# Performance work log

Hardware: AMD Instinct MI355X
Metric: run time of the kernel (lower is better)

Reference implementation:

```python
import math
import jax, jax.numpy as jnp
import numpy as np

B, L, D, H = 4, 512, 256, 8
DH = D // H
BUCKETS = 11  # rel_pos_buckets; padding_idx = BUCKETS


def setup_inputs() -> dict:
    key = jax.random.key(0)
    ks = jax.random.split(key, 12)
    s = 0.02
    rel_table = jax.random.normal(ks[10], (BUCKETS + 1, D), dtype=jnp.float32) * s
    rel_table = rel_table.at[BUCKETS].set(0.0)  # padding_idx row is zero
    return {
        "inputs": jax.random.normal(ks[0], (B, L, D), dtype=jnp.float32),
        "mask": jax.random.randint(ks[1], (B, L, L), 0, 2) > 0,
        "distances": jax.random.randint(ks[2], (B, L, L), 0, BUCKETS + 1),
        "Wq": jax.random.normal(ks[3], (D, D), dtype=jnp.float32) * s,
        "bq": jnp.zeros((D,), jnp.float32),
        "Wk": jax.random.normal(ks[4], (D, D), dtype=jnp.float32) * s,
        "bk": jnp.zeros((D,), jnp.float32),
        "Wv": jax.random.normal(ks[5], (D, D), dtype=jnp.float32) * s,
        "bv": jnp.zeros((D,), jnp.float32),
        "Wo": jax.random.normal(ks[6], (D, D), dtype=jnp.float32) * s,
        "bo": jnp.zeros((D,), jnp.float32),
        "rel_table": rel_table,
        "u": jax.random.normal(ks[7], (D,), dtype=jnp.float32) * s,
        "v": jax.random.normal(ks[8], (D,), dtype=jnp.float32) * s,
    }


def reference(inputs, mask, distances, Wq, bq, Wk, bk, Wv, bv, Wo, bo, rel_table, u, v):
    def shape(x):  # (B, L, D) -> (B, H, L, DH)
        return x.reshape(B, L, H, DH).transpose(0, 2, 1, 3)

    q = shape(inputs @ Wq + bq) / math.sqrt(DH)
    k = shape(inputs @ Wk + bk)
    val = shape(inputs @ Wv + bv)

    # content term: (q + u) k^T
    a_c = jnp.einsum("bhqd,bhkd->bhqk", q + u.reshape(1, H, 1, DH), k)

    # relative-position term: embedding gather (padding row already zero, mask anyway)
    valid = (distances != BUCKETS)[..., None].astype(rel_table.dtype)
    rel = (rel_table[distances] * valid).reshape(B, L, L, H, DH)  # (B, Lq, Lk, H, DH)
    b_d = jnp.einsum("bhqd,bqkhd->bhqk", q + v.reshape(1, H, 1, DH), rel)

    scores = jnp.where(mask[:, None, :, :], jnp.float32(-1e18), a_c + b_d)
    attn = jax.nn.softmax(scores, axis=-1)  # (B, H, Lq, Lk)

    ctx = jnp.einsum("bhqk,bhkd->bhqd", attn, val)
    ctx = ctx.transpose(0, 2, 1, 3).reshape(B, L, D)
    output = ctx @ Wo + bo
    return output, attn
```

## Files before the change

kernel.cpp:

```cpp
#include <hip/hip_runtime.h>
#include <math.h>

#define BB 4
#define LL 512
#define DD 256
#define HH 8
#define DHH 32
#define NB 12

__global__ __launch_bounds__(256) void qkv_kernel(const float* __restrict__ x,
    const float* __restrict__ Wq, const float* __restrict__ bq,
    const float* __restrict__ Wk, const float* __restrict__ bk,
    const float* __restrict__ Wv, const float* __restrict__ bv,
    const float* __restrict__ uvec, const float* __restrict__ vvec,
    float* __restrict__ Qu, float* __restrict__ Qv,
    float* __restrict__ KT, float* __restrict__ V) {
    __shared__ float xs[8][DD];
    const int mat = blockIdx.x >> 8;
    const int r0 = (blockIdx.x & 255) * 8;
    const int t = threadIdx.x;
    const int cg = t & 63, rg = t >> 6;
    const int c0 = cg * 4;
    {
        const float4* xg = (const float4*)(x + r0 * DD);
        float4* xsv = (float4*)&xs[0][0];
        xsv[t] = xg[t];
        xsv[t + 256] = xg[t + 256];
    }
    __syncthreads();
    const float* W    = (mat == 0) ? Wq : (mat == 1) ? Wk : Wv;
    const float* bias = (mat == 0) ? bq : (mat == 1) ? bk : bv;
    float acc[2][4];
#pragma unroll
    for (int r = 0; r < 2; ++r)
#pragma unroll
        for (int c = 0; c < 4; ++c) acc[r][c] = bias[c0 + c];
    for (int i0 = 0; i0 < DD; i0 += 4) {
        float4 wv4[4], xv4[2];
#pragma unroll
        for (int j = 0; j < 4; ++j) wv4[j] = *(const float4*)&W[(i0 + j) * DD + c0];
#pragma unroll
        for (int r = 0; r < 2; ++r) xv4[r] = *(const float4*)&xs[rg * 2 + r][i0];
        const float* wf = (const float*)wv4;
        const float* xf = (const float*)xv4;
#pragma unroll
        for (int r = 0; r < 2; ++r)
#pragma unroll
            for (int j = 0; j < 4; ++j)
#pragma unroll
                for (int c = 0; c < 4; ++c)
                    acc[r][c] = fmaf(xf[r * 4 + j], wf[j * 4 + c], acc[r][c]);
    }
    if (mat == 0) {
        const float s = 0.17677669529663687f;
        const float4 u4 = *(const float4*)&uvec[c0];
        const float4 v4 = *(const float4*)&vvec[c0];
#pragma unroll
        for (int r = 0; r < 2; ++r) {
            const int row = r0 + rg * 2 + r;
            float4 q = make_float4(acc[r][0] * s, acc[r][1] * s, acc[r][2] * s, acc[r][3] * s);
            *(float4*)&Qu[row * DD + c0] = make_float4(q.x + u4.x, q.y + u4.y, q.z + u4.z, q.w + u4.w);
            *(float4*)&Qv[row * DD + c0] = make_float4(q.x + v4.x, q.y + v4.y, q.z + v4.z, q.w + v4.w);
        }
    } else if (mat == 1) {
        const int b = r0 >> 9;
        const int kb = (r0 & 511) + rg * 2;
#pragma unroll
        for (int c = 0; c < 4; ++c) {
            const int col = c0 + c;
            const int h = col >> 5, dd = col & 31;
            float* p = KT + ((long)((b * HH + h) * DHH + dd)) * LL + kb;
            p[0] = acc[0][c];
            p[1] = acc[1][c];
        }
    } else {
#pragma unroll
        for (int r = 0; r < 2; ++r)
            *(float4*)&V[(r0 + rg * 2 + r) * DD + c0] =
                make_float4(acc[r][0], acc[r][1], acc[r][2], acc[r][3]);
    }
}

__global__ __launch_bounds__(512, 4) void scores_ctx_kernel(const float* __restrict__ Qu,
    const float* __restrict__ Qv, const float* __restrict__ KT,
    const float* __restrict__ rel_table, const int* __restrict__ mask,
    const int* __restrict__ dist, const float* __restrict__ V,
    float* __restrict__ attn, float* __restrict__ ctx) {
    __shared__ float Qs[16][DHH];
    __shared__ float Qv8[16][DHH];
    __shared__ float rels[NB][DHH + 1];
    __shared__ float Ps[16][NB];
    __shared__ float Ss[16][4][132];
    __shared__ float Vs[DHH][133];
    const int blk = blockIdx.x;
    const int h = blk & 7;
    const int rest = blk >> 3;
    const int qt = rest & 31;
    const int b = rest >> 5;
    const int q0 = qt * 16;
    const int t = threadIdx.x;
    const int w = t >> 6, l = t & 63;

    {
        const int r = t >> 5, c = t & 31;
        Qs[r][c]  = Qu[(b * LL + q0 + r) * DD + h * DHH + c];
        Qv8[r][c] = Qv[(b * LL + q0 + r) * DD + h * DHH + c];
    }
    if (t < NB * DHH) {
        rels[t >> 5][t & 31] = rel_table[(t >> 5) * DD + h * DHH + (t & 31)];
    }
    __syncthreads();
    if (t < 16 * NB) {
        const int bk = t >> 4, r = t & 15;
        float a = 0.f;
#pragma unroll
        for (int d = 0; d < DHH; ++d) a = fmaf(Qv8[r][d], rels[bk][d], a);
        Ps[r][bk] = a;
    }
    __syncthreads();

    const int r0 = 2 * w;
    const long kbase = (long)(b * HH + h) * DHH * LL;
    float e0[2][4], e1[2][4];
    float sum0 = 0.f, sum1 = 0.f;
#pragma unroll
    for (int s = 0; s < 2; ++s) {
        const int k0 = 4 * l + 256 * s;
        const int4 dx0 = *(const int4*)&dist[(b * LL + q0 + r0) * LL + k0];
        const int4 dx1 = *(const int4*)&dist[(b * LL + q0 + r0 + 1) * LL + k0];
        const int4 mx0 = *(const int4*)&mask[(b * LL + q0 + r0) * LL + k0];
        const int4 mx1 = *(const int4*)&mask[(b * LL + q0 + r0 + 1) * LL + k0];
        float s0[4], s1[4];
        s0[0] = Ps[r0][dx0.x]; s0[1] = Ps[r0][dx0.y]; s0[2] = Ps[r0][dx0.z]; s0[3] = Ps[r0][dx0.w];
        s1[0] = Ps[r0 + 1][dx1.x]; s1[1] = Ps[r0 + 1][dx1.y]; s1[2] = Ps[r0 + 1][dx1.z]; s1[3] = Ps[r0 + 1][dx1.w];
#pragma unroll
        for (int d8 = 0; d8 < DHH; d8 += 8) {
            float4 kv[8];
#pragma unroll
            for (int j = 0; j < 8; ++j)
                kv[j] = *(const float4*)&KT[kbase + (long)(d8 + j) * LL + k0];
            const float4 q0a = *(const float4*)&Qs[r0][d8];
            const float4 q0b = *(const float4*)&Qs[r0][d8 + 4];
            const float4 q1a = *(const float4*)&Qs[r0 + 1][d8];
            const float4 q1b = *(const float4*)&Qs[r0 + 1][d8 + 4];
            const float* qa0 = (const float*)&q0a;
            const float* qb0 = (const float*)&q0b;
            const float* qa1 = (const float*)&q1a;
            const float* qb1 = (const float*)&q1b;
#pragma unroll
            for (int j = 0; j < 4; ++j) {
                s0[0] = fmaf(qa0[j], kv[j].x, s0[0]);
                s0[1] = fmaf(qa0[j], kv[j].y, s0[1]);
                s0[2] = fmaf(qa0[j], kv[j].z, s0[2]);
                s0[3] = fmaf(qa0[j], kv[j].w, s0[3]);
                s1[0] = fmaf(qa1[j], kv[j].x, s1[0]);
                s1[1] = fmaf(qa1[j], kv[j].y, s1[1]);
                s1[2] = fmaf(qa1[j], kv[j].z, s1[2]);
                s1[3] = fmaf(qa1[j], kv[j].w, s1[3]);
            }
#pragma unroll
            for (int j = 0; j < 4; ++j) {
                s0[0] = fmaf(qb0[j], kv[j + 4].x, s0[0]);
                s0[1] = fmaf(qb0[j], kv[j + 4].y, s0[1]);
                s0[2] = fmaf(qb0[j], kv[j + 4].z, s0[2]);
                s0[3] = fmaf(qb0[j], kv[j + 4].w, s0[3]);
                s1[0] = fmaf(qb1[j], kv[j + 4].x, s1[0]);
                s1[1] = fmaf(qb1[j], kv[j + 4].y, s1[1]);
                s1[2] = fmaf(qb1[j], kv[j + 4].z, s1[2]);
                s1[3] = fmaf(qb1[j], kv[j + 4].w, s1[3]);
            }
        }
        e0[s][0] = mx0.x ? 0.f : __expf(s0[0]);
        e0[s][1] = mx0.y ? 0.f : __expf(s0[1]);
        e0[s][2] = mx0.z ? 0.f : __expf(s0[2]);
        e0[s][3] = mx0.w ? 0.f : __expf(s0[3]);
        e1[s][0] = mx1.x ? 0.f : __expf(s1[0]);
        e1[s][1] = mx1.y ? 0.f : __expf(s1[1]);
        e1[s][2] = mx1.z ? 0.f : __expf(s1[2]);
        e1[s][3] = mx1.w ? 0.f : __expf(s1[3]);
        sum0 += (e0[s][0] + e0[s][1]) + (e0[s][2] + e0[s][3]);
        sum1 += (e1[s][0] + e1[s][1]) + (e1[s][2] + e1[s][3]);
    }
    for (int off = 32; off > 0; off >>= 1) {
        sum0 += __shfl_xor(sum0, off);
        sum1 += __shfl_xor(sum1, off);
    }
    const float i0 = 1.0f / sum0, i1 = 1.0f / sum1;
    float* a0 = attn + ((long)(b * HH + h) * LL + q0 + r0) * LL;
    float* a1 = a0 + LL;
#pragma unroll
    for (int s = 0; s < 2; ++s) {
        const int k0 = 4 * l + 256 * s;
        const int ch = k0 >> 7, off = k0 & 127;
        const float4 o0 = make_float4(e0[s][0] * i0, e0[s][1] * i0, e0[s][2] * i0, e0[s][3] * i0);
        const float4 o1 = make_float4(e1[s][0] * i1, e1[s][1] * i1, e1[s][2] * i1, e1[s][3] * i1);
        *(float4*)&a0[k0] = o0;
        *(float4*)&a1[k0] = o1;
        *(float4*)&Ss[r0][ch][off] = o0;
        *(float4*)&Ss[r0 + 1][ch][off] = o1;
    }

    const int qB = t >> 5;
    const int dB = t & 31;
    const int kkS = t >> 2;
    const int dqS = (t & 3) * 8;
    float acc = 0.f;
    for (int c = 0; c < 4; ++c) {
        __syncthreads();
        {
            const float* vg = V + ((long)(b * LL + c * 128 + kkS)) * DD + h * DHH + dqS;
            const float4 va = *(const float4*)&vg[0];
            const float4 vb4 = *(const float4*)&vg[4];
            Vs[dqS + 0][kkS] = va.x;  Vs[dqS + 1][kkS] = va.y;
            Vs[dqS + 2][kkS] = va.z;  Vs[dqS + 3][kkS] = va.w;
            Vs[dqS + 4][kkS] = vb4.x; Vs[dqS + 5][kkS] = vb4.y;
            Vs[dqS + 6][kkS] = vb4.z; Vs[dqS + 7][kkS] = vb4.w;
        }
        __syncthreads();
#pragma unroll
        for (int j = 0; j < 32; ++j) {
            const float4 sv = *(const float4*)&Ss[qB][c][4 * j];
            const float4 vv = *(const float4*)&Vs[dB][4 * j];
            acc = fmaf(sv.x, vv.x, fmaf(sv.y, vv.y, fmaf(sv.z, vv.z, fmaf(sv.w, vv.w, acc))));
        }
    }
    ctx[(b * LL + q0 + qB) * DD + h * DHH + dB] = acc;
}

__global__ __launch_bounds__(256) void outproj_kernel(const float* __restrict__ ctx,
    const float* __restrict__ Wo, const float* __restrict__ bo,
    float* __restrict__ out) {
    __shared__ float xs[4][DD];
    const int r0 = blockIdx.x * 4;
    const int t = threadIdx.x;
    const int rg = t >> 6;
    const int c0 = (t & 63) * 4;
    ((float4*)&xs[0][0])[t] = ((const float4*)(ctx + r0 * DD))[t];
    __syncthreads();
    float4 acc = *(const float4*)&bo[c0];
    for (int i0 = 0; i0 < DD; i0 += 8) {
        float4 wv[8];
#pragma unroll
        for (int j = 0; j < 8; ++j) wv[j] = *(const float4*)&Wo[(i0 + j) * DD + c0];
        const float4 x0 = *(const float4*)&xs[rg][i0];
        const float4 x1 = *(const float4*)&xs[rg][i0 + 4];
        const float* xf0 = (const float*)&x0;
        const float* xf1 = (const float*)&x1;
#pragma unroll
        for (int j = 0; j < 4; ++j) {
            acc.x = fmaf(xf0[j], wv[j].x, acc.x);
            acc.y = fmaf(xf0[j], wv[j].y, acc.y);
            acc.z = fmaf(xf0[j], wv[j].z, acc.z);
            acc.w = fmaf(xf0[j], wv[j].w, acc.w);
        }
#pragma unroll
        for (int j = 0; j < 4; ++j) {
            acc.x = fmaf(xf1[j], wv[j + 4].x, acc.x);
            acc.y = fmaf(xf1[j], wv[j + 4].y, acc.y);
            acc.z = fmaf(xf1[j], wv[j + 4].z, acc.z);
            acc.w = fmaf(xf1[j], wv[j + 4].w, acc.w);
        }
    }
    *(float4*)&out[(r0 + rg) * DD + c0] = acc;
}

extern "C" void kernel_launch(void* const* d_in, const int* in_sizes, int n_in,
                              void* d_out, int out_size, void* d_ws, size_t ws_size,
                              hipStream_t stream) {
    const float* x    = (const float*)d_in[0];
    const int* mk     = (const int*)d_in[1];
    const int* dist   = (const int*)d_in[2];
    const float* Wq = (const float*)d_in[3];
    const float* bq = (const float*)d_in[4];
    const float* Wk = (const float*)d_in[5];
    const float* bk = (const float*)d_in[6];
    const float* Wv = (const float*)d_in[7];
    const float* bv = (const float*)d_in[8];
    const float* Wo = (const float*)d_in[9];
    const float* bo = (const float*)d_in[10];
    const float* rel_table = (const float*)d_in[11];
    const float* uvec = (const float*)d_in[12];
    const float* vvec = (const float*)d_in[13];

    float* out  = (float*)d_out;
    float* attn = out + BB * LL * DD;

    float* Qu = (float*)d_ws;
    float* Qv = Qu + BB * LL * DD;
    float* KT = Qv + BB * LL * DD;
    float* V  = KT + BB * LL * DD;
    float* C  = V + BB * LL * DD;

    qkv_kernel<<<3 * 256, 256, 0, stream>>>(x, Wq, bq, Wk, bk, Wv, bv, uvec, vvec,
                                            Qu, Qv, KT, V);
    scores_ctx_kernel<<<BB * (LL / 16) * HH, 512, 0, stream>>>(Qu, Qv, KT, rel_table,
                                                               mk, dist, V, attn, C);
    outproj_kernel<<<BB * LL / 4, 256, 0, stream>>>(C, Wo, bo, out);
}
```

Baseline: 179.3 us.

## Register-tile P·V with split-K across threads and XOR-swizzled score buffer

```diff
diff --git a/kernel.cpp b/kernel.cpp
--- a/kernel.cpp
+++ b/kernel.cpp
@@ -87,97 +87,108 @@
     const int* __restrict__ dist, const float* __restrict__ V,
     float* __restrict__ attn, float* __restrict__ ctx) {
     __shared__ float Qs[16][DHH];
-    __shared__ float Qv8[16][DHH];
-    __shared__ float rels[NB][DHH + 1];
     __shared__ float Ps[16][NB];
-    __shared__ float Ss[16][4][132];
+    __shared__ float ss[16 * 512];
     __shared__ float Vs[DHH][133];
     const int blk = blockIdx.x;
     const int h = blk & 7;
     const int rest = blk >> 3;
-    const int qt = rest & 31;
+    const int qt16 = rest & 31;
     const int b = rest >> 5;
-    const int q0 = qt * 16;
+    const int q0 = qt16 * 16;
     const int t = threadIdx.x;
     const int w = t >> 6, l = t & 63;
 
+    float* Qv8  = ss;
+    float* rels = ss + 512;
+
     {
         const int r = t >> 5, c = t & 31;
-        Qs[r][c]  = Qu[(b * LL + q0 + r) * DD + h * DHH + c];
-        Qv8[r][c] = Qv[(b * LL + q0 + r) * DD + h * DHH + c];
+        Qs[r][c]          = Qu[(b * LL + q0 + r) * DD + h * DHH + c];
+        Qv8[r * DHH + c]  = Qv[(b * LL + q0 + r) * DD + h * DHH + c];
     }
     if (t < NB * DHH) {
-        rels[t >> 5][t & 31] = rel_table[(t >> 5) * DD + h * DHH + (t & 31)];
+        rels[(t >> 5) * 33 + (t & 31)] = rel_table[(t >> 5) * DD + h * DHH + (t & 31)];
     }
     __syncthreads();
     if (t < 16 * NB) {
         const int bk = t >> 4, r = t & 15;
         float a = 0.f;
 #pragma unroll
-        for (int d = 0; d < DHH; ++d) a = fmaf(Qv8[r][d], rels[bk][d], a);
+        for (int d = 0; d < DHH; ++d) a = fmaf(Qv8[r * DHH + d], rels[bk * 33 + d], a);
         Ps[r][bk] = a;
     }
     __syncthreads();
 
     const int r0 = 2 * w;
     const long kbase = (long)(b * HH + h) * DHH * LL;
-    float e0[2][4], e1[2][4];
-    float sum0 = 0.f, sum1 = 0.f;
+    float sc[2][2][4];
 #pragma unroll
     for (int s = 0; s < 2; ++s) {
         const int k0 = 4 * l + 256 * s;
         const int4 dx0 = *(const int4*)&dist[(b * LL + q0 + r0) * LL + k0];
         const int4 dx1 = *(const int4*)&dist[(b * LL + q0 + r0 + 1) * LL + k0];
+        sc[0][s][0] = Ps[r0][dx0.x];     sc[0][s][1] = Ps[r0][dx0.y];
+        sc[0][s][2] = Ps[r0][dx0.z];     sc[0][s][3] = Ps[r0][dx0.w];
+        sc[1][s][0] = Ps[r0 + 1][dx1.x]; sc[1][s][1] = Ps[r0 + 1][dx1.y];
+        sc[1][s][2] = Ps[r0 + 1][dx1.z]; sc[1][s][3] = Ps[r0 + 1][dx1.w];
+    }
+#pragma unroll
+    for (int d8 = 0; d8 < DHH; d8 += 8) {
+        const float4 q0a = *(const float4*)&Qs[r0][d8];
+        const float4 q0b = *(const float4*)&Qs[r0][d8 + 4];
+        const float4 q1a = *(const float4*)&Qs[r0 + 1][d8];
+        const float4 q1b = *(const float4*)&Qs[r0 + 1][d8 + 4];
+        const float* qa0 = (const float*)&q0a;
+        const float* qb0 = (const float*)&q0b;
+        const float* qa1 = (const float*)&q1a;
+        const float* qb1 = (const float*)&q1b;
+#pragma unroll
+        for (int s = 0; s < 2; ++s) {
+            const int k0 = 4 * l + 256 * s;
+            float4 kv[8];
+#pragma unroll
+            for (int j = 0; j < 8; ++j)
+                kv[j] = *(const float4*)&KT[kbase + (long)(d8 + j) * LL + k0];
+#pragma unroll
+            for (int j = 0; j < 4; ++j) {
+                sc[0][s][0] = fmaf(qa0[j], kv[j].x, sc[0][s][0]);
+                sc[0][s][1] = fmaf(qa0[j], kv[j].y, sc[0][s][1]);
+                sc[0][s][2] = fmaf(qa0[j], kv[j].z, sc[0][s][2]);
+                sc[0][s][3] = fmaf(qa0[j], kv[j].w, sc[0][s][3]);
+                sc[1][s][0] = fmaf(qa1[j], kv[j].x, sc[1][s][0]);
+                sc[1][s][1] = fmaf(qa1[j], kv[j].y, sc[1][s][1]);
+                sc[1][s][2] = fmaf(qa1[j], kv[j].z, sc[1][s][2]);
+                sc[1][s][3] = fmaf(qa1[j], kv[j].w, sc[1][s][3]);
+            }
+#pragma unroll
+            for (int j = 0; j < 4; ++j) {
+                sc[0][s][0] = fmaf(qb0[j], kv[j + 4].x, sc[0][s][0]);
+                sc[0][s][1] = fmaf(qb0[j], kv[j + 4].y, sc[0][s][1]);
+                sc[0][s][2] = fmaf(qb0[j], kv[j + 4].z, sc[0][s][2]);
+                sc[0][s][3] = fmaf(qb0[j], kv[j + 4].w, sc[0][s][3]);
+                sc[1][s][0] = fmaf(qb1[j], kv[j + 4].x, sc[1][s][0]);
+                sc[1][s][1] = fmaf(qb1[j], kv[j + 4].y, sc[1][s][1]);
+                sc[1][s][2] = fmaf(qb1[j], kv[j + 4].z, sc[1][s][2]);
+                sc[1][s][3] = fmaf(qb1[j], kv[j + 4].w, sc[1][s][3]);
+            }
+        }
+    }
+    float e0[2][4], e1[2][4];
+    float sum0 = 0.f, sum1 = 0.f;
+#pragma unroll
+    for (int s = 0; s < 2; ++s) {
+        const int k0 = 4 * l + 256 * s;
         const int4 mx0 = *(const int4*)&mask[(b * LL + q0 + r0) * LL + k0];
         const int4 mx1 = *(const int4*)&mask[(b * LL + q0 + r0 + 1) * LL + k0];
-        float s0[4], s1[4];
-        s0[0] = Ps[r0][dx0.x]; s0[1] = Ps[r0][dx0.y]; s0[2] = Ps[r0][dx0.z]; s0[3] = Ps[r0][dx0.w];
-        s1[0] = Ps[r0 + 1][dx1.x]; s1[1] = Ps[r0 + 1][dx1.y]; s1[2] = Ps[r0 + 1][dx1.z]; s1[3] = Ps[r0 + 1][dx1.w];
-#pragma unroll
-        for (int d8 = 0; d8 < DHH; d8 += 8) {
-            float4 kv[8];
-#pragma unroll
-            for (int j = 0; j < 8; ++j)
-                kv[j] = *(const float4*)&KT[kbase + (long)(d8 + j) * LL + k0];
-            const float4 q0a = *(const float4*)&Qs[r0][d8];
-            const float4 q0b = *(const float4*)&Qs[r0][d8 + 4];
-            const float4 q1a = *(const float4*)&Qs[r0 + 1][d8];
-            const float4 q1b = *(const float4*)&Qs[r0 + 1][d8 + 4];
-            const float* qa0 = (const float*)&q0a;
-            const float* qb0 = (const float*)&q0b;
-            const float* qa1 = (const float*)&q1a;
-            const float* qb1 = (const float*)&q1b;
-#pragma unroll
-            for (int j = 0; j < 4; ++j) {
-                s0[0] = fmaf(qa0[j], kv[j].x, s0[0]);
-                s0[1] = fmaf(qa0[j], kv[j].y, s0[1]);
-                s0[2] = fmaf(qa0[j], kv[j].z, s0[2]);
-                s0[3] = fmaf(qa0[j], kv[j].w, s0[3]);
-                s1[0] = fmaf(qa1[j], kv[j].x, s1[0]);
-                s1[1] = fmaf(qa1[j], kv[j].y, s1[1]);
-                s1[2] = fmaf(qa1[j], kv[j].z, s1[2]);
-                s1[3] = fmaf(qa1[j], kv[j].w, s1[3]);
-            }
-#pragma unroll
-            for (int j = 0; j < 4; ++j) {
-                s0[0] = fmaf(qb0[j], kv[j + 4].x, s0[0]);
-                s0[1] = fmaf(qb0[j], kv[j + 4].y, s0[1]);
-                s0[2] = fmaf(qb0[j], kv[j + 4].z, s0[2]);
-                s0[3] = fmaf(qb0[j], kv[j + 4].w, s0[3]);
-                s1[0] = fmaf(qb1[j], kv[j + 4].x, s1[0]);
-                s1[1] = fmaf(qb1[j], kv[j + 4].y, s1[1]);
-                s1[2] = fmaf(qb1[j], kv[j + 4].z, s1[2]);
-                s1[3] = fmaf(qb1[j], kv[j + 4].w, s1[3]);
-            }
-        }
-        e0[s][0] = mx0.x ? 0.f : __expf(s0[0]);
-        e0[s][1] = mx0.y ? 0.f : __expf(s0[1]);
-        e0[s][2] = mx0.z ? 0.f : __expf(s0[2]);
-        e0[s][3] = mx0.w ? 0.f : __expf(s0[3]);
-        e1[s][0] = mx1.x ? 0.f : __expf(s1[0]);
-        e1[s][1] = mx1.y ? 0.f : __expf(s1[1]);
-        e1[s][2] = mx1.z ? 0.f : __expf(s1[2]);
-        e1[s][3] = mx1.w ? 0.f : __expf(s1[3]);
+        e0[s][0] = mx0.x ? 0.f : __expf(sc[0][s][0]);
+        e0[s][1] = mx0.y ? 0.f : __expf(sc[0][s][1]);
+        e0[s][2] = mx0.z ? 0.f : __expf(sc[0][s][2]);
+        e0[s][3] = mx0.w ? 0.f : __expf(sc[0][s][3]);
+        e1[s][0] = mx1.x ? 0.f : __expf(sc[1][s][0]);
+        e1[s][1] = mx1.y ? 0.f : __expf(sc[1][s][1]);
+        e1[s][2] = mx1.z ? 0.f : __expf(sc[1][s][2]);
+        e1[s][3] = mx1.w ? 0.f : __expf(sc[1][s][3]);
         sum0 += (e0[s][0] + e0[s][1]) + (e0[s][2] + e0[s][3]);
         sum1 += (e1[s][0] + e1[s][1]) + (e1[s][2] + e1[s][3]);
     }
@@ -185,26 +196,33 @@
         sum0 += __shfl_xor(sum0, off);
         sum1 += __shfl_xor(sum1, off);
     }
-    const float i0 = 1.0f / sum0, i1 = 1.0f / sum1;
+    const float inv0 = 1.0f / sum0, inv1 = 1.0f / sum1;
     float* a0 = attn + ((long)(b * HH + h) * LL + q0 + r0) * LL;
     float* a1 = a0 + LL;
 #pragma unroll
     for (int s = 0; s < 2; ++s) {
         const int k0 = 4 * l + 256 * s;
-        const int ch = k0 >> 7, off = k0 & 127;
-        const float4 o0 = make_float4(e0[s][0] * i0, e0[s][1] * i0, e0[s][2] * i0, e0[s][3] * i0);
-        const float4 o1 = make_float4(e1[s][0] * i1, e1[s][1] * i1, e1[s][2] * i1, e1[s][3] * i1);
+        const int ch = k0 >> 7;
+        const int oct = (k0 & 127) >> 3;
+        const int h4 = k0 & 4;
+        const float4 o0 = make_float4(e0[s][0] * inv0, e0[s][1] * inv0, e0[s][2] * inv0, e0[s][3] * inv0);
+        const float4 o1 = make_float4(e1[s][0] * inv1, e1[s][1] * inv1, e1[s][2] * inv1, e1[s][3] * inv1);
         *(float4*)&a0[k0] = o0;
         *(float4*)&a1[k0] = o1;
-        *(float4*)&Ss[r0][ch][off] = o0;
-        *(float4*)&Ss[r0 + 1][ch][off] = o1;
-    }
-
-    const int qB = t >> 5;
-    const int dB = t & 31;
+        *(float4*)&ss[r0 * 512 + ch * 128 + (((oct ^ r0) << 3) | h4)] = o0;
+        *(float4*)&ss[(r0 + 1) * 512 + ch * 128 + (((oct ^ (r0 + 1)) << 3) | h4)] = o1;
+    }
+
+    const int qt = t & 3;
+    const int dt = (t >> 2) & 7;
+    const int kg = t >> 5;
     const int kkS = t >> 2;
     const int dqS = (t & 3) * 8;
-    float acc = 0.f;
+    float acc[4][4];
+#pragma unroll
+    for (int i = 0; i < 4; ++i)
+#pragma unroll
+        for (int jd = 0; jd < 4; ++jd) acc[i][jd] = 0.f;
     for (int c = 0; c < 4; ++c) {
         __syncthreads();
         {
@@ -218,13 +236,37 @@
         }
         __syncthreads();
 #pragma unroll
-        for (int j = 0; j < 32; ++j) {
-            const float4 sv = *(const float4*)&Ss[qB][c][4 * j];
-            const float4 vv = *(const float4*)&Vs[dB][4 * j];
-            acc = fmaf(sv.x, vv.x, fmaf(sv.y, vv.y, fmaf(sv.z, vv.z, fmaf(sv.w, vv.w, acc))));
-        }
-    }
-    ctx[(b * LL + q0 + qB) * DD + h * DHH + dB] = acc;
+        for (int ki = 0; ki < 2; ++ki) {
+            float4 vv[4], sv[4];
+#pragma unroll
+            for (int jd = 0; jd < 4; ++jd)
+                vv[jd] = *(const float4*)&Vs[dt * 4 + jd][(kg << 3) | (ki << 2)];
+#pragma unroll
+            for (int i = 0; i < 4; ++i) {
+                const int q = qt * 4 + i;
+                sv[i] = *(const float4*)&ss[q * 512 + c * 128 + (((kg ^ q) << 3) | (ki << 2))];
+            }
+#pragma unroll
+            for (int i = 0; i < 4; ++i)
+#pragma unroll
+                for (int jd = 0; jd < 4; ++jd)
+                    acc[i][jd] = fmaf(sv[i].x, vv[jd].x, fmaf(sv[i].y, vv[jd].y,
+                                 fmaf(sv[i].z, vv[jd].z, fmaf(sv[i].w, vv[jd].w, acc[i][jd]))));
+        }
+    }
+    __syncthreads();
+#pragma unroll
+    for (int i = 0; i < 4; ++i)
+        *(float4*)&ss[kg * 512 + (qt * 4 + i) * 32 + dt * 4] =
+            make_float4(acc[i][0], acc[i][1], acc[i][2], acc[i][3]);
+    __syncthreads();
+    {
+        const int qr = t >> 5, dr = t & 31;
+        float r = 0.f;
+#pragma unroll
+        for (int kg2 = 0; kg2 < 16; ++kg2) r += ss[kg2 * 512 + qr * 32 + dr];
+        ctx[(b * LL + q0 + qr) * DD + h * DHH + dr] = r;
+    }
 }
 
 __global__ __launch_bounds__(256) void outproj_kernel(const float* __restrict__ ctx,
```

New measurement: 444.5 us. 2.48x slower.

## Register-tile attn·V product with split-K partials and XOR-swizzled score buffer

Applied to the files above, without the earlier changes.

```diff
diff --git a/kernel.cpp b/kernel.cpp
--- a/kernel.cpp
+++ b/kernel.cpp
@@ -87,34 +87,35 @@
     const int* __restrict__ dist, const float* __restrict__ V,
     float* __restrict__ attn, float* __restrict__ ctx) {
     __shared__ float Qs[16][DHH];
-    __shared__ float Qv8[16][DHH];
-    __shared__ float rels[NB][DHH + 1];
     __shared__ float Ps[16][NB];
-    __shared__ float Ss[16][4][132];
+    __shared__ float ss[16 * 512];
     __shared__ float Vs[DHH][133];
     const int blk = blockIdx.x;
     const int h = blk & 7;
     const int rest = blk >> 3;
-    const int qt = rest & 31;
+    const int qt16 = rest & 31;
     const int b = rest >> 5;
-    const int q0 = qt * 16;
+    const int q0 = qt16 * 16;
     const int t = threadIdx.x;
     const int w = t >> 6, l = t & 63;
 
+    float* Qv8  = ss;
+    float* rels = ss + 512;
+
     {
         const int r = t >> 5, c = t & 31;
-        Qs[r][c]  = Qu[(b * LL + q0 + r) * DD + h * DHH + c];
-        Qv8[r][c] = Qv[(b * LL + q0 + r) * DD + h * DHH + c];
+        Qs[r][c]          = Qu[(b * LL + q0 + r) * DD + h * DHH + c];
+        Qv8[r * DHH + c]  = Qv[(b * LL + q0 + r) * DD + h * DHH + c];
     }
     if (t < NB * DHH) {
-        rels[t >> 5][t & 31] = rel_table[(t >> 5) * DD + h * DHH + (t & 31)];
+        rels[(t >> 5) * 33 + (t & 31)] = rel_table[(t >> 5) * DD + h * DHH + (t & 31)];
     }
     __syncthreads();
     if (t < 16 * NB) {
         const int bk = t >> 4, r = t & 15;
         float a = 0.f;
 #pragma unroll
-        for (int d = 0; d < DHH; ++d) a = fmaf(Qv8[r][d], rels[bk][d], a);
+        for (int d = 0; d < DHH; ++d) a = fmaf(Qv8[r * DHH + d], rels[bk * 33 + d], a);
         Ps[r][bk] = a;
     }
     __syncthreads();
@@ -185,26 +186,34 @@
         sum0 += __shfl_xor(sum0, off);
         sum1 += __shfl_xor(sum1, off);
     }
-    const float i0 = 1.0f / sum0, i1 = 1.0f / sum1;
+    const float inv0 = 1.0f / sum0, inv1 = 1.0f / sum1;
     float* a0 = attn + ((long)(b * HH + h) * LL + q0 + r0) * LL;
     float* a1 = a0 + LL;
 #pragma unroll
     for (int s = 0; s < 2; ++s) {
         const int k0 = 4 * l + 256 * s;
-        const int ch = k0 >> 7, off = k0 & 127;
-        const float4 o0 = make_float4(e0[s][0] * i0, e0[s][1] * i0, e0[s][2] * i0, e0[s][3] * i0);
-        const float4 o1 = make_float4(e1[s][0] * i1, e1[s][1] * i1, e1[s][2] * i1, e1[s][3] * i1);
+        const int ch = k0 >> 7;
+        const int oct = (k0 & 127) >> 3;
+        const int h4 = k0 & 4;
+        const float4 o0 = make_float4(e0[s][0] * inv0, e0[s][1] * inv0, e0[s][2] * inv0, e0[s][3] * inv0);
+        const float4 o1 = make_float4(e1[s][0] * inv1, e1[s][1] * inv1, e1[s][2] * inv1, e1[s][3] * inv1);
         *(float4*)&a0[k0] = o0;
         *(float4*)&a1[k0] = o1;
-        *(float4*)&Ss[r0][ch][off] = o0;
-        *(float4*)&Ss[r0 + 1][ch][off] = o1;
-    }
-
-    const int qB = t >> 5;
-    const int dB = t & 31;
+        *(float4*)&ss[r0 * 512 + ch * 128 + (((oct ^ (r0 >> 2)) << 3) | h4)] = o0;
+        *(float4*)&ss[(r0 + 1) * 512 + ch * 128 + (((oct ^ ((r0 + 1) >> 2)) << 3) | h4)] = o1;
+    }
+
+    const int qt = t & 3;
+    const int dt = (t >> 2) & 7;
+    const int kg = t >> 5;
     const int kkS = t >> 2;
     const int dqS = (t & 3) * 8;
-    float acc = 0.f;
+    float acc[4][4];
+#pragma unroll
+    for (int i = 0; i < 4; ++i)
+#pragma unroll
+        for (int jd = 0; jd < 4; ++jd) acc[i][jd] = 0.f;
+#pragma unroll 1
     for (int c = 0; c < 4; ++c) {
         __syncthreads();
         {
@@ -218,13 +227,34 @@
         }
         __syncthreads();
 #pragma unroll
-        for (int j = 0; j < 32; ++j) {
-            const float4 sv = *(const float4*)&Ss[qB][c][4 * j];
-            const float4 vv = *(const float4*)&Vs[dB][4 * j];
-            acc = fmaf(sv.x, vv.x, fmaf(sv.y, vv.y, fmaf(sv.z, vv.z, fmaf(sv.w, vv.w, acc))));
-        }
-    }
-    ctx[(b * LL + q0 + qB) * DD + h * DHH + dB] = acc;
+        for (int ki = 0; ki < 2; ++ki) {
+            float4 sv[4];
+#pragma unroll
+            for (int i = 0; i < 4; ++i)
+                sv[i] = *(const float4*)&ss[(qt * 4 + i) * 512 + c * 128 + (((kg ^ qt) << 3) | (ki << 2))];
+#pragma unroll
+            for (int jd = 0; jd < 4; ++jd) {
+                const float4 vv = *(const float4*)&Vs[dt * 4 + jd][(kg << 3) | (ki << 2)];
+#pragma unroll
+                for (int i = 0; i < 4; ++i)
+                    acc[i][jd] = fmaf(sv[i].x, vv.x, fmaf(sv[i].y, vv.y,
+                                 fmaf(sv[i].z, vv.z, fmaf(sv[i].w, vv.w, acc[i][jd]))));
+            }
+        }
+    }
+    __syncthreads();
+#pragma unroll
+    for (int i = 0; i < 4; ++i)
+        *(float4*)&ss[kg * 512 + (qt * 4 + i) * 32 + dt * 4] =
+            make_float4(acc[i][0], acc[i][1], acc[i][2], acc[i][3]);
+    __syncthreads();
+    {
+        const int qr = t >> 5, dr = t & 31;
+        float r = 0.f;
+#pragma unroll
+        for (int kg2 = 0; kg2 < 16; ++kg2) r += ss[kg2 * 512 + qr * 32 + dr];
+        ctx[(b * LL + q0 + qr) * DD + h * DHH + dr] = r;
+    }
 }
 
 __global__ __launch_bounds__(256) void outproj_kernel(const float* __restrict__ ctx,
```

After: 170.1 us. -5.1%, faster.
